# Kernel optimization log

Measured on AMD Instinct MI355X. Metric: run time of the kernel, lower is better.

Reference implementation:

```python
import jax, jax.numpy as jnp
import numpy as np
from jax import lax

B, L, D = 2, 1024, 1024
N_LAYER, D_STATE, D_CONV = 4, 16, 4
E = 2 * D          # d_inner (expand=2)
DT_RANK = (D + 15) // 16
EPS = 1e-5


def rmsnorm(x, w):
    v = jnp.mean(jnp.square(x), axis=-1, keepdims=True)
    return x * lax.rsqrt(v + EPS) * w


def setup_inputs() -> dict:
    key = jax.random.key(0)
    ks = jax.random.split(key, 8)
    s = 0.02
    A_log = jnp.broadcast_to(jnp.log(jnp.arange(1, D_STATE + 1, dtype=jnp.float32)),
                             (N_LAYER, E, D_STATE)) + 0.0
    return {
        "hidden_states": jax.random.normal(ks[0], (B, L, D), jnp.float32),
        "in_proj_w": jax.random.normal(ks[1], (N_LAYER, 2 * E, D), jnp.float32) * s,
        "conv_w": jax.random.normal(ks[2], (N_LAYER, E, D_CONV), jnp.float32) * 0.2,
        "conv_b": jnp.zeros((N_LAYER, E), jnp.float32),
        "x_proj_w": jax.random.normal(ks[3], (N_LAYER, DT_RANK + 2 * D_STATE, E), jnp.float32) * s,
        "dt_proj_w": jax.random.normal(ks[4], (N_LAYER, E, DT_RANK), jnp.float32) * 0.1,
        "dt_proj_b": jnp.full((N_LAYER, E), -4.6, jnp.float32),  # softplus -> ~0.01
        "A_log": A_log,
        "D_param": jnp.ones((N_LAYER, E), jnp.float32),
        "out_proj_w": jax.random.normal(ks[5], (N_LAYER, D, E), jnp.float32) * s,
        "norm_w": jnp.ones((N_LAYER, D), jnp.float32),
        "norm_f_w": jnp.ones((D,), jnp.float32),
    }


def mamba_mixer(x, ipw, cw, cb, xpw, dtw, dtb, A_log, Dp, opw):
    # x: (B,L,D)
    xz = jnp.einsum('bld,ed->ble', x, ipw)          # (B,L,2E)
    xi, z = jnp.split(xz, 2, axis=-1)               # each (B,L,E)
    # causal depthwise conv over time
    xt = jnp.moveaxis(xi, 1, 2)                     # (B,E,L)
    xc = lax.conv_general_dilated(xt, cw[:, None, :], (1,), [(D_CONV - 1, 0)],
                                  feature_group_count=E,
                                  dimension_numbers=('NCH', 'OIH', 'NCH'))
    xc = jax.nn.silu(xc + cb[None, :, None])
    u = jnp.moveaxis(xc, 1, 2)                      # (B,L,E)
    # input-dependent dt, B, C
    xdb = jnp.einsum('ble,re->blr', u, xpw)         # (B,L,DT_RANK+2N)
    dt_in, Bm, C = jnp.split(xdb, [DT_RANK, DT_RANK + D_STATE], axis=-1)
    dt = jax.nn.softplus(jnp.einsum('blr,er->ble', dt_in, dtw) + dtb)  # (B,L,E)
    A = -jnp.exp(A_log)                             # (E,N)

    def step(h, inp):
        dt_t, B_t, C_t, u_t = inp                   # (B,E),(B,N),(B,N),(B,E)
        dA = jnp.exp(dt_t[..., None] * A)           # (B,E,N)
        h = dA * h + (dt_t * u_t)[..., None] * B_t[:, None, :]
        return h, jnp.einsum('ben,bn->be', h, C_t)

    h0 = jnp.zeros((x.shape[0], E, D_STATE), x.dtype)
    xs = (jnp.moveaxis(dt, 1, 0), jnp.moveaxis(Bm, 1, 0),
          jnp.moveaxis(C, 1, 0), jnp.moveaxis(u, 1, 0))
    _, ys = lax.scan(step, h0, xs)                  # ys: (L,B,E)
    y = jnp.moveaxis(ys, 0, 1) + u * Dp
    y = y * jax.nn.silu(z)
    return jnp.einsum('ble,de->bld', y, opw)


def reference(hidden_states, in_proj_w, conv_w, conv_b, x_proj_w, dt_proj_w,
              dt_proj_b, A_log, D_param, out_proj_w, norm_w, norm_f_w):
    h, residual = hidden_states, None
    for i in range(N_LAYER):
        residual = h if residual is None else h + residual  # fused add
        hn = rmsnorm(residual, norm_w[i])                   # prenorm
        h = mamba_mixer(hn, in_proj_w[i], conv_w[i], conv_b[i], x_proj_w[i],
                        dt_proj_w[i], dt_proj_b[i], A_log[i], D_param[i], out_proj_w[i])
    # final fused add + RMSNorm (prenorm=False)
    return rmsnorm(h + residual, norm_f_w)
```

## Files before the change

kernel.cpp:

```cpp
#include <hip/hip_runtime.h>
#include <hip/hip_bf16.h>
#include <math.h>

namespace {
constexpr int Bb = 2, Ll = 1024, Dd = 1024;
constexpr int NLAYER = 4, DSTATE = 16, DCONV = 4;
constexpr int Ee = 2 * Dd;
constexpr int DTRANK = (Dd + 15) / 16;
constexpr int XPROJ = DTRANK + 2 * DSTATE;
constexpr float EPS = 1e-5f;
constexpr int ROWS = Bb * Ll;
constexpr int SCH = 32;
constexpr int SCL = Ll / SCH;
}

typedef short bf16x8 __attribute__((ext_vector_type(8)));
typedef float f32x4  __attribute__((ext_vector_type(4)));
typedef unsigned short us8 __attribute__((ext_vector_type(8)));

__device__ __forceinline__ float ldin(const void* p, size_t i, int isbf) {
    if (isbf) return __bfloat162float(((const __hip_bfloat16*)p)[i]);
    return ((const float*)p)[i];
}

__device__ __forceinline__ float b2f(__hip_bfloat16 x) { return __bfloat162float(x); }

__device__ __forceinline__ unsigned short f2bf(float f) {
    union { float f; unsigned u; } x; x.f = f;
    const unsigned r = x.u + 0x7FFFu + ((x.u >> 16) & 1u);
    return (unsigned short)(r >> 16);
}

__global__ void detect_kernel(const unsigned* __restrict__ nf, int* __restrict__ flag) {
    if (threadIdx.x == 0 && blockIdx.x == 0)
        *flag = (nf[0] == 0x3F800000u) ? 0 : 1;
}

__global__ __launch_bounds__(256) void zero_kernel(float* __restrict__ p, int n) {
    const int i = blockIdx.x * 256 + threadIdx.x;
    if (i < n) p[i] = 0.f;
}

__global__ __launch_bounds__(256) void wconv_kernel(
    const void* __restrict__ src, size_t off, unsigned short* __restrict__ dst,
    int n, const int* __restrict__ flagp)
{
    const int isbf = *flagp;
    const int i = (blockIdx.x * 256 + threadIdx.x) * 8;
    if (i >= n) return;
    us8 h;
    if (isbf) {
        h = *(const us8*)((const unsigned short*)src + off + i);
    } else {
        const float* sp = (const float*)src + off + i;
        const float4 v0 = *(const float4*)sp;
        const float4 v1 = *(const float4*)(sp + 4);
        h[0] = f2bf(v0.x); h[1] = f2bf(v0.y); h[2] = f2bf(v0.z); h[3] = f2bf(v0.w);
        h[4] = f2bf(v1.x); h[5] = f2bf(v1.y); h[6] = f2bf(v1.z); h[7] = f2bf(v1.w);
    }
    *(us8*)(dst + i) = h;
}

__global__ __launch_bounds__(256) void addnorm_kernel(
    const void* __restrict__ h_in, const float* __restrict__ h_f,
    float* __restrict__ res, const void* __restrict__ w, size_t w_off,
    __hip_bfloat16* __restrict__ hn_out, void* __restrict__ out, int mode,
    const int* __restrict__ flagp)
{
    const int isbf = *flagp;
    const int row = blockIdx.x;
    const int tid = threadIdx.x;
    const size_t base = (size_t)row * Dd;

    float vals[4];
    float ssum = 0.f;
#pragma unroll
    for (int i = 0; i < 4; i++) {
        const int d = tid + i * 256;
        float v;
        if (mode == 0) v = ldin(h_in, base + d, isbf);
        else           v = res[base + d] + h_f[base + d];
        vals[i] = v;
        ssum += v * v;
    }
#pragma unroll
    for (int off = 32; off > 0; off >>= 1) ssum += __shfl_down(ssum, off, 64);
    __shared__ float sred[4];
    if ((tid & 63) == 0) sred[tid >> 6] = ssum;
    __syncthreads();
    const float tot = sred[0] + sred[1] + sred[2] + sred[3];
    const float scale = rsqrtf(tot / (float)Dd + EPS);

#pragma unroll
    for (int i = 0; i < 4; i++) {
        const int d = tid + i * 256;
        const float v = vals[i];
        const float o = v * scale * ldin(w, w_off + d, isbf);
        if (mode == 2) {
            if (isbf) ((__hip_bfloat16*)out)[base + d] = __float2bfloat16(o);
            else      ((float*)out)[base + d] = o;
        } else {
            res[base + d] = v;
            hn_out[base + d] = __float2bfloat16(o);
        }
    }
}

template<int BM, int BN, int WGM, int WGN, bool ABF, int CMODE>
__global__ __launch_bounds__(256) void gemm_mfma_t(
    const void* __restrict__ Abase, int lda,
    const unsigned short* __restrict__ W,
    void* __restrict__ Cout, int M, int N, int K, int Kc,
    const void* __restrict__ bias, size_t bias_off,
    const int* __restrict__ flagp)
{
    constexpr int BK = 64, BKP = 72;
    constexpr int FM = (BM / WGM) / 16;
    constexpr int FN = (BN / WGN) / 16;
    constexpr int PA = BM / 32;
    constexpr int PW = BN / 32;
    __shared__ __align__(16) unsigned short As[BM][BKP];
    __shared__ __align__(16) unsigned short Bs[BN][BKP];

    const int tid = threadIdx.x;
    const int m0 = blockIdx.y * BM, n0 = blockIdx.x * BN;
    const int kbeg = blockIdx.z * Kc;
    const int kend = (kbeg + Kc < K) ? (kbeg + Kc) : K;

    const int srow = tid >> 3;
    const int scol = (tid & 7) * 8;

    us8 ra[PA], rw[PW];

    auto loadA = [&](int k0) {
#pragma unroll
        for (int p = 0; p < PA; p++) {
            const int row = p * 32 + srow;
            if constexpr (ABF) {
                ra[p] = *(const us8*)((const unsigned short*)Abase +
                         (size_t)(m0 + row) * lda + k0 + scol);
            } else {
                const float* ap = (const float*)Abase + (size_t)(m0 + row) * lda + k0 + scol;
                const float4 v0 = *(const float4*)ap;
                const float4 v1 = *(const float4*)(ap + 4);
                us8 h;
                h[0] = f2bf(v0.x); h[1] = f2bf(v0.y); h[2] = f2bf(v0.z); h[3] = f2bf(v0.w);
                h[4] = f2bf(v1.x); h[5] = f2bf(v1.y); h[6] = f2bf(v1.z); h[7] = f2bf(v1.w);
                ra[p] = h;
            }
        }
    };
    auto loadW = [&](int k0) {
#pragma unroll
        for (int p = 0; p < PW; p++) {
            const int n = p * 32 + srow;
            us8 h = (us8)0;
            if (n0 + n < N)
                h = *(const us8*)(W + (size_t)(n0 + n) * K + k0 + scol);
            rw[p] = h;
        }
    };

    const int wave = tid >> 6, lane = tid & 63;
    const int wm = (wave / WGN) * FM * 16;
    const int wn = (wave % WGN) * FN * 16;
    const int quad = lane >> 4, l16 = lane & 15;

    f32x4 acc[FM][FN];
#pragma unroll
    for (int i = 0; i < FM; i++)
#pragma unroll
        for (int j = 0; j < FN; j++)
            acc[i][j] = (f32x4){0.f, 0.f, 0.f, 0.f};

    loadA(kbeg);
    loadW(kbeg);
    for (int k0 = kbeg; k0 < kend; k0 += BK) {
#pragma unroll
        for (int p = 0; p < PA; p++) *(us8*)&As[p * 32 + srow][scol] = ra[p];
#pragma unroll
        for (int p = 0; p < PW; p++) *(us8*)&Bs[p * 32 + srow][scol] = rw[p];
        __syncthreads();
        if (k0 + BK < kend) { loadA(k0 + BK); loadW(k0 + BK); }
#pragma unroll
        for (int kk = 0; kk < 2; kk++) {
            bf16x8 af[FM], bw[FN];
#pragma unroll
            for (int i = 0; i < FM; i++)
                af[i] = *(const bf16x8*)&As[wm + i * 16 + l16][kk * 32 + quad * 8];
#pragma unroll
            for (int j = 0; j < FN; j++)
                bw[j] = *(const bf16x8*)&Bs[wn + j * 16 + l16][kk * 32 + quad * 8];
#pragma unroll
            for (int i = 0; i < FM; i++)
#pragma unroll
                for (int j = 0; j < FN; j++)
                    acc[i][j] = __builtin_amdgcn_mfma_f32_16x16x32_bf16(
                        af[i], bw[j], acc[i][j], 0, 0, 0);
        }
        __syncthreads();
    }

#pragma unroll
    for (int j = 0; j < FN; j++) {
        const int gn = n0 + wn + j * 16 + l16;
        if (gn >= N) continue;
        float bv = 0.f;
        if constexpr (CMODE == 4) bv = ldin(bias, bias_off + gn, *flagp);
#pragma unroll
        for (int i = 0; i < FM; i++) {
            const int gm = m0 + wm + i * 16 + quad * 4;
#pragma unroll
            for (int r = 0; r < 4; r++) {
                float v = acc[i][j][r];
                const size_t ci = (size_t)(gm + r) * N + gn;
                if constexpr (CMODE == 3) {
                    atomicAdd((float*)Cout + ci, v);
                } else if constexpr (CMODE == 2) {
                    ((__hip_bfloat16*)Cout)[ci] = __float2bfloat16(v);
                } else if constexpr (CMODE == 4) {
                    v += bv;
                    v = (v > 20.f) ? v : log1pf(expf(v));
                    ((__hip_bfloat16*)Cout)[ci] = __float2bfloat16(v);
                } else {
                    ((float*)Cout)[ci] = v;
                }
            }
        }
    }
}

__global__ __launch_bounds__(256) void conv_kernel(
    const __hip_bfloat16* __restrict__ xz,
    const void* __restrict__ cw, size_t cw_off,
    const void* __restrict__ cb, size_t cb_off,
    __hip_bfloat16* __restrict__ u, const int* __restrict__ flagp)
{
    const int isbf = *flagp;
    const int idx = blockIdx.x * 256 + threadIdx.x;
    const int e = idx & (Ee - 1);
    const int bl = idx >> 11;
    const int l = bl & (Ll - 1);

    float acc = ldin(cb, cb_off + e, isbf);
#pragma unroll
    for (int k = 0; k < DCONV; k++) {
        const int ls = l - (DCONV - 1) + k;
        if (ls >= 0) {
            const float x = b2f(xz[(size_t)(bl - (DCONV - 1) + k) * (2 * Ee) + e]);
            acc = fmaf(ldin(cw, cw_off + e * DCONV + k, isbf), x, acc);
        }
    }
    const float s = acc / (1.f + __expf(-acc));
    u[idx] = __float2bfloat16(s);
}

__global__ __launch_bounds__(256) void scan_part1(
    const __hip_bfloat16* __restrict__ dt, const __hip_bfloat16* __restrict__ u,
    const float* __restrict__ xdb,
    const void* __restrict__ A_log, size_t al_off,
    float* __restrict__ hend, float* __restrict__ Ssum,
    const int* __restrict__ flagp)
{
    const int isbf = *flagp;
    const int blk = blockIdx.x;
    const int b   = blk >> 8;
    const int c   = (blk >> 3) & (SCH - 1);
    const int e   = ((blk & 7) << 8) + threadIdx.x;

    float A[DSTATE], h[DSTATE];
#pragma unroll
    for (int n = 0; n < DSTATE; n++) {
        A[n] = -__expf(ldin(A_log, al_off + (size_t)e * DSTATE + n, isbf));
        h[n] = 0.f;
    }
    float S = 0.f;
    const int l0 = c * SCL;
    const __hip_bfloat16* dt_p = dt + ((size_t)b * Ll + l0) * Ee + e;
    const __hip_bfloat16* u_p  = u  + ((size_t)b * Ll + l0) * Ee + e;
    const float* bc_p = xdb + ((size_t)b * Ll + l0) * XPROJ + DTRANK;

#pragma unroll 2
    for (int l = 0; l < SCL; l++) {
        const float dtv = b2f(dt_p[(size_t)l * Ee]);
        const float uv  = b2f(u_p[(size_t)l * Ee]);
        const float du  = dtv * uv;
        S += dtv;
#pragma unroll
        for (int n = 0; n < DSTATE; n++)
            h[n] = fmaf(__expf(dtv * A[n]), h[n], du * bc_p[(size_t)l * XPROJ + n]);
    }
    const size_t hb = (size_t)(b * SCH + c) * DSTATE * Ee + e;
#pragma unroll
    for (int n = 0; n < DSTATE; n++)
        hend[hb + (size_t)n * Ee] = h[n];
    Ssum[(size_t)(b * SCH + c) * Ee + e] = S;
}

__global__ __launch_bounds__(256) void scan_part2(
    const float* __restrict__ Ssum, float* __restrict__ hh,
    const void* __restrict__ A_log, size_t al_off,
    const int* __restrict__ flagp)
{
    const int isbf = *flagp;
    const int idx = blockIdx.x * 256 + threadIdx.x;
    const int e = idx & (Ee - 1);
    const int n = (idx >> 11) & (DSTATE - 1);
    const int b = idx >> 15;
    const float A = -__expf(ldin(A_log, al_off + (size_t)e * DSTATE + n, isbf));
    float h = 0.f;
    for (int c = 0; c < SCH; c++) {
        const size_t off = ((size_t)(b * SCH + c) * DSTATE + n) * Ee + e;
        const float a  = __expf(A * Ssum[(size_t)(b * SCH + c) * Ee + e]);
        const float he = hh[off];
        hh[off] = h;
        h = fmaf(a, h, he);
    }
}

__global__ __launch_bounds__(256) void scan_part3(
    const __hip_bfloat16* __restrict__ dt, const __hip_bfloat16* __restrict__ u,
    const float* __restrict__ xdb, const __hip_bfloat16* __restrict__ xz,
    const float* __restrict__ hinit,
    const void* __restrict__ A_log, size_t al_off,
    const void* __restrict__ Dp, size_t dp_off,
    __hip_bfloat16* __restrict__ y, const int* __restrict__ flagp)
{
    const int isbf = *flagp;
    const int blk = blockIdx.x;
    const int b   = blk >> 8;
    const int c   = (blk >> 3) & (SCH - 1);
    const int e   = ((blk & 7) << 8) + threadIdx.x;

    float A[DSTATE], h[DSTATE];
    const size_t hb = (size_t)(b * SCH + c) * DSTATE * Ee + e;
#pragma unroll
    for (int n = 0; n < DSTATE; n++) {
        A[n] = -__expf(ldin(A_log, al_off + (size_t)e * DSTATE + n, isbf));
        h[n] = hinit[hb + (size_t)n * Ee];
    }
    const float De = ldin(Dp, dp_off + e, isbf);
    const int l0 = c * SCL;
    const __hip_bfloat16* dt_p = dt + ((size_t)b * Ll + l0) * Ee + e;
    const __hip_bfloat16* u_p  = u  + ((size_t)b * Ll + l0) * Ee + e;
    const __hip_bfloat16* z_p  = xz + ((size_t)b * Ll + l0) * (2 * Ee) + Ee + e;
    const float* bc_p = xdb + ((size_t)b * Ll + l0) * XPROJ + DTRANK;
    __hip_bfloat16* y_p = y + ((size_t)b * Ll + l0) * Ee + e;

#pragma unroll 2
    for (int l = 0; l < SCL; l++) {
        const float dtv = b2f(dt_p[(size_t)l * Ee]);
        const float uv  = b2f(u_p[(size_t)l * Ee]);
        const float zv  = b2f(z_p[(size_t)l * 2 * Ee]);
        const float du  = dtv * uv;
        float acc = 0.f;
#pragma unroll
        for (int n = 0; n < DSTATE; n++) {
            h[n] = fmaf(__expf(dtv * A[n]), h[n], du * bc_p[(size_t)l * XPROJ + n]);
            acc = fmaf(h[n], bc_p[(size_t)l * XPROJ + DSTATE + n], acc);
        }
        const float sz = zv / (1.f + __expf(-zv));
        y_p[(size_t)l * Ee] = __float2bfloat16(fmaf(uv, De, acc) * sz);
    }
}

extern "C" void kernel_launch(void* const* d_in, const int* in_sizes, int n_in,
                              void* d_out, int out_size, void* d_ws, size_t ws_size,
                              hipStream_t stream)
{
    const void* hs    = d_in[0];
    const void* ipw   = d_in[1];
    const void* convw = d_in[2];
    const void* convb = d_in[3];
    const void* xpw   = d_in[4];
    const void* dtw   = d_in[5];
    const void* dtb   = d_in[6];
    const void* alog  = d_in[7];
    const void* dpar  = d_in[8];
    const void* opw   = d_in[9];
    const void* normw = d_in[10];
    const void* normf = d_in[11];

    int*   flag = (int*)d_ws;
    float* res  = (float*)d_ws + 64;
    float* hf   = res  + (size_t)ROWS * Dd;
    float* xdb  = hf   + (size_t)ROWS * Dd;
    float* hend = xdb  + (size_t)ROWS * XPROJ;
    float* Ssum = hend + (size_t)Bb * SCH * DSTATE * Ee;
    __hip_bfloat16* hn = (__hip_bfloat16*)(Ssum + (size_t)Bb * SCH * Ee);
    __hip_bfloat16* xz = hn + (size_t)ROWS * Dd;
    __hip_bfloat16* u  = xz + (size_t)ROWS * 2 * Ee;
    __hip_bfloat16* y  = u  + (size_t)ROWS * Ee;
    __hip_bfloat16* dt = y  + (size_t)ROWS * Ee;
    unsigned short* wip = (unsigned short*)(dt + (size_t)ROWS * Ee);
    unsigned short* wxp = wip + (size_t)2 * Ee * Dd;
    unsigned short* wdt = wxp + (size_t)XPROJ * Ee;
    unsigned short* wop = wdt + (size_t)Ee * DTRANK;

    const size_t need_bytes =
        4 * (64 + (size_t)ROWS * Dd * 2 + (size_t)ROWS * XPROJ +
             (size_t)Bb * SCH * DSTATE * Ee + (size_t)Bb * SCH * Ee) +
        2 * ((size_t)ROWS * Dd + (size_t)ROWS * 2 * Ee + (size_t)ROWS * Ee * 3) +
        2 * ((size_t)2 * Ee * Dd + (size_t)XPROJ * Ee + (size_t)Ee * DTRANK +
             (size_t)Dd * Ee);
    if (need_bytes > ws_size) return;

    detect_kernel<<<1, 64, 0, stream>>>((const unsigned*)normf, flag);

    for (int i = 0; i < NLAYER; i++) {
        {
            const int nip = 2 * Ee * Dd, nxp = XPROJ * Ee,
                      ndt = Ee * DTRANK, nop = Dd * Ee;
            wconv_kernel<<<nip / (256 * 8), 256, 0, stream>>>(
                ipw, (size_t)i * nip, wip, nip, flag);
            wconv_kernel<<<nxp / (256 * 8), 256, 0, stream>>>(
                xpw, (size_t)i * nxp, wxp, nxp, flag);
            wconv_kernel<<<ndt / (256 * 8), 256, 0, stream>>>(
                dtw, (size_t)i * ndt, wdt, ndt, flag);
            wconv_kernel<<<nop / (256 * 8), 256, 0, stream>>>(
                opw, (size_t)i * nop, wop, nop, flag);
        }

        addnorm_kernel<<<ROWS, 256, 0, stream>>>(
            hs, hf, res, normw, (size_t)i * Dd, hn, nullptr, i == 0 ? 0 : 1, flag);

        {
            dim3 g(2 * Ee / 64, ROWS / 128, 1);
            gemm_mfma_t<128, 64, 4, 1, true, 2><<<g, 256, 0, stream>>>(
                hn, Dd, wip, xz, ROWS, 2 * Ee, Dd, Dd, nullptr, 0, flag);
        }

        conv_kernel<<<ROWS * Ee / 256, 256, 0, stream>>>(
            xz, convw, (size_t)i * Ee * DCONV, convb, (size_t)i * Ee, u, flag);

        zero_kernel<<<(ROWS * XPROJ + 255) / 256, 256, 0, stream>>>(
            xdb, ROWS * XPROJ);
        {
            dim3 g(2, ROWS / 64, 8);
            gemm_mfma_t<64, 64, 2, 2, true, 3><<<g, 256, 0, stream>>>(
                u, Ee, wxp, xdb, ROWS, XPROJ, Ee, Ee / 8, nullptr, 0, flag);
        }

        {
            dim3 g(Ee / 64, ROWS / 128, 1);
            gemm_mfma_t<128, 64, 4, 1, false, 4><<<g, 256, 0, stream>>>(
                xdb, XPROJ, wdt, dt, ROWS, Ee, DTRANK, DTRANK,
                dtb, (size_t)i * Ee, flag);
        }

        scan_part1<<<Bb * SCH * (Ee / 256), 256, 0, stream>>>(
            dt, u, xdb, alog, (size_t)i * Ee * DSTATE, hend, Ssum, flag);
        scan_part2<<<Bb * DSTATE * Ee / 256, 256, 0, stream>>>(
            Ssum, hend, alog, (size_t)i * Ee * DSTATE, flag);
        scan_part3<<<Bb * SCH * (Ee / 256), 256, 0, stream>>>(
            dt, u, xdb, xz, hend, alog, (size_t)i * Ee * DSTATE,
            dpar, (size_t)i * Ee, y, flag);

        {
            dim3 g(Dd / 64, ROWS / 64, 1);
            gemm_mfma_t<64, 64, 2, 2, true, 0><<<g, 256, 0, stream>>>(
                y, Ee, wop, hf, ROWS, Dd, Ee, Ee, nullptr, 0, flag);
        }
    }

    addnorm_kernel<<<ROWS, 256, 0, stream>>>(
        nullptr, hf, res, normf, 0, nullptr, d_out, 2, flag);
}
```

Baseline: 835.1 us.

## Double-buffer GEMM LDS tiles with two-deep prefetch and XCD-aware block remap

The MFMA GEMM now keeps two LDS buffers per operand. Each iteration stages the next tile into the alternate buffer and issues global loads two tiles ahead, which cuts the per-iteration barriers from two to one and overlaps global and LDS traffic with MFMA work. It also remaps block indices so consecutive row tiles land on the same XCD, aiming for better L2 reuse of the A rows. The cost is doubled LDS use, which may lower occupancy, plus more live registers for the prefetched tile.

Measured after the change: 846.3 us. No clear change (+1.3%).

```diff
diff --git a/kernel.cpp b/kernel.cpp
--- a/kernel.cpp
+++ b/kernel.cpp
@@ -119,11 +119,23 @@
     constexpr int FN = (BN / WGN) / 16;
     constexpr int PA = BM / 32;
     constexpr int PW = BN / 32;
-    __shared__ __align__(16) unsigned short As[BM][BKP];
-    __shared__ __align__(16) unsigned short Bs[BN][BKP];
+    __shared__ __align__(16) unsigned short As[2][BM][BKP];
+    __shared__ __align__(16) unsigned short Bs[2][BN][BKP];
 
     const int tid = threadIdx.x;
-    const int m0 = blockIdx.y * BM, n0 = blockIdx.x * BN;
+
+    int bx = blockIdx.x, by = blockIdx.y;
+    {
+        const int gx = gridDim.x, gy = gridDim.y;
+        if ((gy & 7) == 0) {
+            const int flat = by * gx + bx;
+            const int xcd = flat & 7;
+            const int q = flat >> 3;
+            by = xcd * (gy >> 3) + q / gx;
+            bx = q % gx;
+        }
+    }
+    const int m0 = by * BM, n0 = bx * BN;
     const int kbeg = blockIdx.z * Kc;
     const int kend = (kbeg + Kc < K) ? (kbeg + Kc) : K;
 
@@ -160,6 +172,12 @@
             rw[p] = h;
         }
     };
+    auto stage = [&](int buf) {
+#pragma unroll
+        for (int p = 0; p < PA; p++) *(us8*)&As[buf][p * 32 + srow][scol] = ra[p];
+#pragma unroll
+        for (int p = 0; p < PW; p++) *(us8*)&Bs[buf][p * 32 + srow][scol] = rw[p];
+    };
 
     const int wave = tid >> 6, lane = tid & 63;
     const int wm = (wave / WGN) * FM * 16;
@@ -173,32 +191,47 @@
         for (int j = 0; j < FN; j++)
             acc[i][j] = (f32x4){0.f, 0.f, 0.f, 0.f};
 
-    loadA(kbeg);
-    loadW(kbeg);
+    loadA(kbeg); loadW(kbeg);
+    stage(0);
+    if (kbeg + BK < kend) { loadA(kbeg + BK); loadW(kbeg + BK); }
+    __syncthreads();
+
+    int cur = 0;
     for (int k0 = kbeg; k0 < kend; k0 += BK) {
-#pragma unroll
-        for (int p = 0; p < PA; p++) *(us8*)&As[p * 32 + srow][scol] = ra[p];
-#pragma unroll
-        for (int p = 0; p < PW; p++) *(us8*)&Bs[p * 32 + srow][scol] = rw[p];
+        bf16x8 af0[FM], bw0[FN];
+#pragma unroll
+        for (int i = 0; i < FM; i++)
+            af0[i] = *(const bf16x8*)&As[cur][wm + i * 16 + l16][quad * 8];
+#pragma unroll
+        for (int j = 0; j < FN; j++)
+            bw0[j] = *(const bf16x8*)&Bs[cur][wn + j * 16 + l16][quad * 8];
+
+        if (k0 + BK < kend) stage(cur ^ 1);
+        if (k0 + 2 * BK < kend) { loadA(k0 + 2 * BK); loadW(k0 + 2 * BK); }
+
+#pragma unroll
+        for (int i = 0; i < FM; i++)
+#pragma unroll
+            for (int j = 0; j < FN; j++)
+                acc[i][j] = __builtin_amdgcn_mfma_f32_16x16x32_bf16(
+                    af0[i], bw0[j], acc[i][j], 0, 0, 0);
+
+        bf16x8 af1[FM], bw1[FN];
+#pragma unroll
+        for (int i = 0; i < FM; i++)
+            af1[i] = *(const bf16x8*)&As[cur][wm + i * 16 + l16][32 + quad * 8];
+#pragma unroll
+        for (int j = 0; j < FN; j++)
+            bw1[j] = *(const bf16x8*)&Bs[cur][wn + j * 16 + l16][32 + quad * 8];
+#pragma unroll
+        for (int i = 0; i < FM; i++)
+#pragma unroll
+            for (int j = 0; j < FN; j++)
+                acc[i][j] = __builtin_amdgcn_mfma_f32_16x16x32_bf16(
+                    af1[i], bw1[j], acc[i][j], 0, 0, 0);
+
         __syncthreads();
-        if (k0 + BK < kend) { loadA(k0 + BK); loadW(k0 + BK); }
-#pragma unroll
-        for (int kk = 0; kk < 2; kk++) {
-            bf16x8 af[FM], bw[FN];
-#pragma unroll
-            for (int i = 0; i < FM; i++)
-                af[i] = *(const bf16x8*)&As[wm + i * 16 + l16][kk * 32 + quad * 8];
-#pragma unroll
-            for (int j = 0; j < FN; j++)
-                bw[j] = *(const bf16x8*)&Bs[wn + j * 16 + l16][kk * 32 + quad * 8];
-#pragma unroll
-            for (int i = 0; i < FM; i++)
-#pragma unroll
-                for (int j = 0; j < FN; j++)
-                    acc[i][j] = __builtin_amdgcn_mfma_f32_16x16x32_bf16(
-                        af[i], bw[j], acc[i][j], 0, 0, 0);
-        }
-        __syncthreads();
+        cur ^= 1;
     }
 
 #pragma unroll
```
